# Performance work log

Measured on AMD Instinct MI355X. Metric: run time of the kernel, lower is better.

## Reference

```python
import jax, jax.numpy as jnp
import numpy as np

LOOKBACK = 1
LOOKAHEAD = 0
SEQ, BATCH, IN, HID = 1024, 16, 1024, 1024
K = LOOKBACK + 1 + LOOKAHEAD


def quick_gelu(x):
    return x * jax.nn.sigmoid(1.702 * x)


def setup_inputs() -> dict:
    key = jax.random.key(0)
    ks = jax.random.split(key, 5)
    scale = 1.0 / np.sqrt(IN * K)  # like torch Conv1d default init scale
    X = jax.random.normal(ks[0], (SEQ, BATCH, IN), dtype=jnp.float32)
    Wz = jax.random.normal(ks[1], (HID, IN, K), dtype=jnp.float32) * scale
    bz = jax.random.normal(ks[2], (HID,), dtype=jnp.float32) * scale
    Wf = jax.random.normal(ks[3], (HID, IN, K), dtype=jnp.float32) * scale
    bf = jax.random.normal(ks[4], (HID,), dtype=jnp.float32) * scale
    return {"X": X, "Wz": Wz, "bz": bz, "Wf": Wf, "bf": bf}


def _conv1d(x_pad, W, b):
    # x_pad: (B, Cin, T+K-1), W: (Cout, Cin, K) -> (B, Cout, T)
    y = jax.lax.conv_general_dilated(
        x_pad, W, window_strides=(1,), padding="VALID",
        dimension_numbers=("NCH", "OIH", "NCH"))
    return y + b[None, :, None]


def reference(X, Wz, bz, Wf, bf):
    # pad time dim: lookback zeros before, lookahead zeros after
    X_pad = jnp.pad(X, ((LOOKBACK, LOOKAHEAD), (0, 0), (0, 0)))
    X_pad = jnp.transpose(X_pad, (1, 2, 0))  # (B, Cin, T+K-1)
    Z = jnp.transpose(_conv1d(X_pad, Wz, bz), (2, 0, 1))  # (T, B, H)
    F = jnp.transpose(_conv1d(X_pad, Wf, bf), (2, 0, 1))  # (T, B, H)
    Z = quick_gelu(Z)
    F = jax.nn.sigmoid(F)

    def step(h, fz):
        f, z = fz
        h = f * z + (1.0 - f) * h
        return h, h

    h0 = jnp.zeros((BATCH, HID), dtype=X.dtype)
    _, H = jax.lax.scan(step, h0, (F, Z))  # H: (T, B, HID)
    return H, H[-1:, :, :]
```

## Files before the change

kernel.cpp:

```cpp
#include <hip/hip_runtime.h>
#include <stdint.h>

#define T_SEQ 1024
#define B_SZ  16
#define C_IN  1024
#define C_HID 1024
#define M_ROWS (T_SEQ * B_SZ)
#define N_COLS (2 * C_HID)
#define K_DIM  (2 * C_IN)

#define NCHUNK 16
#define CLEN   (T_SEQ / NCHUNK)
#define NBH    (B_SZ * C_HID)

typedef __attribute__((ext_vector_type(8))) short bf16x8;
typedef __attribute__((ext_vector_type(4))) float f32x4;
typedef unsigned short u16;

#define MFMA __builtin_amdgcn_mfma_f32_16x16x32_bf16

__device__ __forceinline__ u16 f2bf(float f) {
  union { float f; unsigned u; } v; v.f = f;
  unsigned r = v.u + 0x7fffu + ((v.u >> 16) & 1u);
  return (u16)(r >> 16);
}
__device__ __forceinline__ float bf2f(unsigned s) {
  union { unsigned u; float f; } v; v.u = s << 16;
  return v.f;
}

__device__ __forceinline__ void async_cp16(const u16* g, u16* l) {
  __builtin_amdgcn_global_load_lds(
      (const __attribute__((address_space(1))) unsigned*)(uintptr_t)g,
      (__attribute__((address_space(3))) unsigned*)(uintptr_t)l,
      16, 0, 0);
}

__global__ void k_convert_x(const float* __restrict__ X, u16* __restrict__ Xp) {
  int i = blockIdx.x * 256 + threadIdx.x;
  const int total4 = (M_ROWS + B_SZ) * C_IN / 4;
  if (i >= total4) return;
  int e = i << 2;
  const int PAD = B_SZ * C_IN;
  ushort4 o;
  if (e < PAD) {
    o.x = o.y = o.z = o.w = 0;
  } else {
    float4 v = *reinterpret_cast<const float4*>(X + (e - PAD));
    o.x = f2bf(v.x); o.y = f2bf(v.y); o.z = f2bf(v.z); o.w = f2bf(v.w);
  }
  *reinterpret_cast<ushort4*>(Xp + e) = o;
}

__global__ void k_repack_w(const float* __restrict__ Wz, const float* __restrict__ Wf,
                           u16* __restrict__ Wt) {
  int i = blockIdx.x * 256 + threadIdx.x;
  if (i >= 2 * 1024 * 1024) return;
  int g  = i >> 20;
  int hc = i & ((1 << 20) - 1);
  int h  = hc >> 10;
  int c  = hc & 1023;
  const float* W = g ? Wf : Wz;
  float2 w = *reinterpret_cast<const float2*>(W + ((size_t)(h << 10) + c) * 2);
  size_t n = ((size_t)h << 1) | (size_t)g;
  Wt[n * K_DIM + c]        = f2bf(w.x);
  Wt[n * K_DIM + 1024 + c] = f2bf(w.y);
}

__global__ __launch_bounds__(512, 2) void k_gemm8(const u16* __restrict__ Xp,
                                                  const u16* __restrict__ Wt,
                                                  const float* __restrict__ bz,
                                                  const float* __restrict__ bfv,
                                                  u16* __restrict__ Cb) {
  __shared__ u16 lds[2][2][2][8192];
  const int tid  = threadIdx.x;
  const int lane = tid & 63;
  const int wid  = tid >> 6;
  const int wr = wid >> 2;
  const int wc = wid & 3;
  const int lr = lane & 15;

  int wg = (blockIdx.x & 7) * 64 + (blockIdx.x >> 3);
  const int m0 = (wg >> 3) << 8;
  const int n0 = (wg & 7) << 8;

  const int p    = tid << 4;
  const int q    = p ^ (((p >> 7) & 7) << 4);
  const int grow = q >> 7;
  const int gcol = (q & 127) >> 1;
  const int ldsw = (tid >> 6) << 9;

  const int rbase = lr << 6;
  int co[2];
#pragma unroll
  for (int ks = 0; ks < 2; ++ks)
    co[ks] = ((((ks << 6) | ((lane >> 4) << 4)) ^ ((lr & 7) << 4)) >> 1);

  auto stage = [&](int j) {
    int kt = j >> 2, part = j & 3, buf = kt & 1;
    if (part >= 2) {
      int h = part - 2;
      const u16* g = Xp + (size_t)(m0 + (h << 7) + grow + ((kt >= 16) ? B_SZ : 0)) * C_IN
                        + ((kt & 15) << 6) + gcol;
      u16* l = &lds[buf][0][h][ldsw];
      async_cp16(g, l);
      async_cp16(g + (size_t)64 * C_IN, l + 4096);
    } else {
      const u16* g = Wt + (size_t)(n0 + (part << 7) + grow) * K_DIM + (kt << 6) + gcol;
      u16* l = &lds[buf][1][part][ldsw];
      async_cp16(g, l);
      async_cp16(g + (size_t)64 * K_DIM, l + 4096);
    }
  };

  f32x4 acc[8][4] = {};
  bf16x8 a[4][2], b0[2][2], b1[2][2];

  for (int j = 0; j < 7; ++j) stage(j);
  asm volatile("s_waitcnt vmcnt(6)" ::: "memory");
  __builtin_amdgcn_s_barrier();

#pragma unroll 2
  for (int t = 0; t < 32; ++t) {
    const int buf = t & 1;
    const u16* pA = &lds[buf][0][wr][0];
    const u16* pB = &lds[buf][1][wc >> 1][(wc & 1) << 12];
    const int jb = 4 * t + 7;

#pragma unroll
    for (int mi = 0; mi < 4; ++mi)
#pragma unroll
      for (int ks = 0; ks < 2; ++ks)
        a[mi][ks] = *(const bf16x8*)(pA + (mi << 10) + rbase + co[ks]);
#pragma unroll
    for (int ni = 0; ni < 2; ++ni)
#pragma unroll
      for (int ks = 0; ks < 2; ++ks)
        b0[ni][ks] = *(const bf16x8*)(pB + (ni << 10) + rbase + co[ks]);
    if (jb < 128) stage(jb);
    __builtin_amdgcn_s_barrier();
    asm volatile("s_waitcnt lgkmcnt(0)" ::: "memory");
    __builtin_amdgcn_s_setprio(1);
#pragma unroll
    for (int mi = 0; mi < 4; ++mi)
#pragma unroll
      for (int ni = 0; ni < 2; ++ni)
#pragma unroll
        for (int ks = 0; ks < 2; ++ks)
          acc[mi][ni] = MFMA(a[mi][ks], b0[ni][ks], acc[mi][ni], 0, 0, 0);
    __builtin_amdgcn_s_setprio(0);
    __builtin_amdgcn_s_barrier();

#pragma unroll
    for (int ni = 0; ni < 2; ++ni)
#pragma unroll
      for (int ks = 0; ks < 2; ++ks)
        b1[ni][ks] = *(const bf16x8*)(pB + ((2 + ni) << 10) + rbase + co[ks]);
    if (jb + 1 < 128) stage(jb + 1);
    __builtin_amdgcn_s_barrier();
    asm volatile("s_waitcnt lgkmcnt(0)" ::: "memory");
    __builtin_amdgcn_s_setprio(1);
#pragma unroll
    for (int mi = 0; mi < 4; ++mi)
#pragma unroll
      for (int ni = 0; ni < 2; ++ni)
#pragma unroll
        for (int ks = 0; ks < 2; ++ks)
          acc[mi][2 + ni] = MFMA(a[mi][ks], b1[ni][ks], acc[mi][2 + ni], 0, 0, 0);
    __builtin_amdgcn_s_setprio(0);
    __builtin_amdgcn_s_barrier();

#pragma unroll
    for (int mi = 0; mi < 4; ++mi)
#pragma unroll
      for (int ks = 0; ks < 2; ++ks)
        a[mi][ks] = *(const bf16x8*)(pA + ((4 + mi) << 10) + rbase + co[ks]);
    if (jb + 2 < 128) stage(jb + 2);
    __builtin_amdgcn_s_barrier();
    asm volatile("s_waitcnt lgkmcnt(0)" ::: "memory");
    __builtin_amdgcn_s_setprio(1);
#pragma unroll
    for (int mi = 0; mi < 4; ++mi)
#pragma unroll
      for (int ni = 0; ni < 2; ++ni)
#pragma unroll
        for (int ks = 0; ks < 2; ++ks)
          acc[4 + mi][2 + ni] = MFMA(a[mi][ks], b1[ni][ks], acc[4 + mi][2 + ni], 0, 0, 0);
    __builtin_amdgcn_s_setprio(0);
    __builtin_amdgcn_s_barrier();

    if (jb + 3 < 128) stage(jb + 3);
    if (t < 30) asm volatile("s_waitcnt vmcnt(6)" ::: "memory");
    else        asm volatile("s_waitcnt vmcnt(0)" ::: "memory");
    __builtin_amdgcn_s_barrier();
    __builtin_amdgcn_s_setprio(1);
#pragma unroll
    for (int mi = 0; mi < 4; ++mi)
#pragma unroll
      for (int ni = 0; ni < 2; ++ni)
#pragma unroll
        for (int ks = 0; ks < 2; ++ks)
          acc[4 + mi][ni] = MFMA(a[mi][ks], b0[ni][ks], acc[4 + mi][ni], 0, 0, 0);
    __builtin_amdgcn_s_setprio(0);
    __builtin_amdgcn_s_barrier();
  }

  const int erow = (lane >> 4) << 2;
  const int ecol = lane & 15;
#pragma unroll
  for (int ni = 0; ni < 4; ++ni) {
    int col  = n0 + (wc << 6) + (ni << 4) + ecol;
    int hcol = col >> 1;
    bool isz = (col & 1) == 0;
    float bias = isz ? bz[hcol] : bfv[hcol];
    float kk   = isz ? 1.702f : 1.0f;
#pragma unroll
    for (int mi = 0; mi < 8; ++mi) {
      int row = m0 + (wr << 7) + (mi << 4) + erow;
#pragma unroll
      for (int r = 0; r < 4; ++r) {
        float v = acc[mi][ni][r] + bias;
        float s = 1.f / (1.f + __expf(-kk * v));
        float res = isz ? v * s : s;
        Cb[(size_t)(row + r) * N_COLS + col] = f2bf(res);
      }
    }
  }
}

__global__ __launch_bounds__(256) void k_scan1(const u16* __restrict__ Cb,
                                               float* __restrict__ Ap,
                                               float* __restrict__ Bp) {
  int i = blockIdx.x * 256 + threadIdx.x;
  int h = i & (C_HID - 1);
  int b = (i >> 10) & (B_SZ - 1);
  int c = i >> 14;
  const unsigned* Cu = (const unsigned*)Cb;
  size_t base = (size_t)b * C_HID + h + (size_t)c * CLEN * NBH;
  float hh = 0.f, P = 1.f;
#pragma unroll 16
  for (int t = 0; t < CLEN; ++t) {
    unsigned zf = Cu[base + (size_t)t * NBH];
    float z = bf2f(zf & 0xffffu);
    float f = bf2f(zf >> 16);
    hh += f * (z - hh);
    P  *= (1.f - f);
  }
  Ap[i] = hh;
  Bp[i] = P;
}

__global__ __launch_bounds__(256) void k_scan2(const float* __restrict__ Ap,
                                               const float* __restrict__ Bp,
                                               float* __restrict__ St) {
  int i = blockIdx.x * 256 + threadIdx.x;
  float hh = 0.f;
#pragma unroll
  for (int c = 0; c < NCHUNK; ++c) {
    St[c * NBH + i] = hh;
    hh = Ap[c * NBH + i] + Bp[c * NBH + i] * hh;
  }
}

__global__ __launch_bounds__(256) void k_scan3(const u16* __restrict__ Cb,
                                               const float* __restrict__ St,
                                               float* __restrict__ out) {
  int i = blockIdx.x * 256 + threadIdx.x;
  int bh = i & (NBH - 1);
  int c = i >> 14;
  const unsigned* Cu = (const unsigned*)Cb;
  size_t base = (size_t)bh + (size_t)c * CLEN * NBH;
  float hh = St[i];
#pragma unroll 16
  for (int t = 0; t < CLEN; ++t) {
    unsigned zf = Cu[base + (size_t)t * NBH];
    float z = bf2f(zf & 0xffffu);
    float f = bf2f(zf >> 16);
    hh += f * (z - hh);
    out[base + (size_t)t * NBH] = hh;
  }
  if (c == NCHUNK - 1)
    out[(size_t)M_ROWS * C_HID + bh] = hh;
}

extern "C" void kernel_launch(void* const* d_in, const int* in_sizes, int n_in,
                              void* d_out, int out_size, void* d_ws, size_t ws_size,
                              hipStream_t stream) {
  const float* X   = (const float*)d_in[0];
  const float* Wz  = (const float*)d_in[1];
  const float* bz  = (const float*)d_in[2];
  const float* Wf  = (const float*)d_in[3];
  const float* bf_ = (const float*)d_in[4];
  float* out = (float*)d_out;

  u16* Xp = (u16*)d_ws;
  u16* Wt = Xp + (size_t)(M_ROWS + B_SZ) * C_IN;
  u16* Cb = Wt + (size_t)N_COLS * K_DIM;
  float* Ap = (float*)Xp;
  float* Bp = Ap + NCHUNK * NBH;
  float* St = Bp + NCHUNK * NBH;

  hipLaunchKernelGGL(k_convert_x, dim3(16400), dim3(256), 0, stream, X, Xp);
  hipLaunchKernelGGL(k_repack_w, dim3(8192), dim3(256), 0, stream, Wz, Wf, Wt);
  hipLaunchKernelGGL(k_gemm8, dim3((M_ROWS / 256) * (N_COLS / 256)), dim3(512), 0,
                     stream, Xp, Wt, bz, bf_, Cb);
  hipLaunchKernelGGL(k_scan1, dim3(NCHUNK * NBH / 256), dim3(256), 0, stream,
                     Cb, Ap, Bp);
  hipLaunchKernelGGL(k_scan2, dim3(NBH / 256), dim3(256), 0, stream, Ap, Bp, St);
  hipLaunchKernelGGL(k_scan3, dim3(NCHUNK * NBH / 256), dim3(256), 0, stream,
                     Cb, St, out);
}
```

Baseline: 308.1 us.

## Store GEMM output in MFMA fragment layout and vectorize scan reads

```diff
diff --git a/kernel.cpp b/kernel.cpp
--- a/kernel.cpp
+++ b/kernel.cpp
@@ -205,25 +205,26 @@
     __builtin_amdgcn_s_barrier();
   }
 
-  const int erow = (lane >> 4) << 2;
-  const int ecol = lane & 15;
+  const int colp = lane & 15;
+  const bool isz = (colp & 1) == 0;
+  const float kk = isz ? 1.702f : 1.0f;
+  const int hbase = (n0 + (wc << 6) + colp) >> 1;
+  const int fmb = (m0 >> 4) + (wr << 3);
+  const int fnb = (n0 >> 4) + (wc << 2);
 #pragma unroll
   for (int ni = 0; ni < 4; ++ni) {
-    int col  = n0 + (wc << 6) + (ni << 4) + ecol;
-    int hcol = col >> 1;
-    bool isz = (col & 1) == 0;
-    float bias = isz ? bz[hcol] : bfv[hcol];
-    float kk   = isz ? 1.702f : 1.0f;
+    float bias = isz ? bz[hbase + 8 * ni] : bfv[hbase + 8 * ni];
 #pragma unroll
     for (int mi = 0; mi < 8; ++mi) {
-      int row = m0 + (wr << 7) + (mi << 4) + erow;
+      ushort4 o;
 #pragma unroll
       for (int r = 0; r < 4; ++r) {
         float v = acc[mi][ni][r] + bias;
         float s = 1.f / (1.f + __expf(-kk * v));
-        float res = isz ? v * s : s;
-        Cb[(size_t)(row + r) * N_COLS + col] = f2bf(res);
+        ((u16*)&o)[r] = f2bf(isz ? v * s : s);
       }
+      size_t fi = (size_t)(fmb + mi) * 128 + (fnb + ni);
+      *reinterpret_cast<ushort4*>(Cb + fi * 256 + (lane << 2)) = o;
     }
   }
 }
@@ -232,33 +233,42 @@
                                                float* __restrict__ Ap,
                                                float* __restrict__ Bp) {
   int i = blockIdx.x * 256 + threadIdx.x;
-  int h = i & (C_HID - 1);
-  int b = (i >> 10) & (B_SZ - 1);
-  int c = i >> 14;
-  const unsigned* Cu = (const unsigned*)Cb;
-  size_t base = (size_t)b * C_HID + h + (size_t)c * CLEN * NBH;
-  float hh = 0.f, P = 1.f;
-#pragma unroll 16
-  for (int t = 0; t < CLEN; ++t) {
-    unsigned zf = Cu[base + (size_t)t * NBH];
-    float z = bf2f(zf & 0xffffu);
-    float f = bf2f(zf >> 16);
-    hh += f * (z - hh);
-    P  *= (1.f - f);
-  }
-  Ap[i] = hh;
-  Bp[i] = P;
+  int h  = i & (C_HID - 1);
+  int b4 = (i >> 10) & 3;
+  int c  = i >> 12;
+  const size_t lane_off = (size_t)(h >> 3) * 256 + b4 * 64 + (h & 7) * 8;
+  float hh[4] = {0.f, 0.f, 0.f, 0.f}, P[4] = {1.f, 1.f, 1.f, 1.f};
+#pragma unroll 8
+  for (int tt = 0; tt < CLEN; ++tt) {
+    size_t t = (size_t)c * CLEN + tt;
+    uint4 v = *reinterpret_cast<const uint4*>(Cb + t * 32768 + lane_off);
+    float z[4] = {bf2f(v.x & 0xffffu), bf2f(v.x >> 16),
+                  bf2f(v.y & 0xffffu), bf2f(v.y >> 16)};
+    float f[4] = {bf2f(v.z & 0xffffu), bf2f(v.z >> 16),
+                  bf2f(v.w & 0xffffu), bf2f(v.w >> 16)};
+#pragma unroll
+    for (int r = 0; r < 4; ++r) {
+      hh[r] += f[r] * (z[r] - hh[r]);
+      P[r]  *= (1.f - f[r]);
+    }
+  }
+  *reinterpret_cast<f32x4*>(Ap + (size_t)i * 4) = (f32x4){hh[0], hh[1], hh[2], hh[3]};
+  *reinterpret_cast<f32x4*>(Bp + (size_t)i * 4) = (f32x4){P[0], P[1], P[2], P[3]};
 }
 
 __global__ __launch_bounds__(256) void k_scan2(const float* __restrict__ Ap,
                                                const float* __restrict__ Bp,
                                                float* __restrict__ St) {
-  int i = blockIdx.x * 256 + threadIdx.x;
-  float hh = 0.f;
+  int j = blockIdx.x * 256 + threadIdx.x;
+  float hh[4] = {0.f, 0.f, 0.f, 0.f};
 #pragma unroll
   for (int c = 0; c < NCHUNK; ++c) {
-    St[c * NBH + i] = hh;
-    hh = Ap[c * NBH + i] + Bp[c * NBH + i] * hh;
+    size_t idx = ((size_t)c * 4096 + j) * 4;
+    *reinterpret_cast<f32x4*>(St + idx) = (f32x4){hh[0], hh[1], hh[2], hh[3]};
+    f32x4 A = *reinterpret_cast<const f32x4*>(Ap + idx);
+    f32x4 B = *reinterpret_cast<const f32x4*>(Bp + idx);
+#pragma unroll
+    for (int r = 0; r < 4; ++r) hh[r] = A[r] + B[r] * hh[r];
   }
 }
 
@@ -266,21 +276,32 @@
                                                const float* __restrict__ St,
                                                float* __restrict__ out) {
   int i = blockIdx.x * 256 + threadIdx.x;
-  int bh = i & (NBH - 1);
-  int c = i >> 14;
-  const unsigned* Cu = (const unsigned*)Cb;
-  size_t base = (size_t)bh + (size_t)c * CLEN * NBH;
-  float hh = St[i];
-#pragma unroll 16
-  for (int t = 0; t < CLEN; ++t) {
-    unsigned zf = Cu[base + (size_t)t * NBH];
-    float z = bf2f(zf & 0xffffu);
-    float f = bf2f(zf >> 16);
-    hh += f * (z - hh);
-    out[base + (size_t)t * NBH] = hh;
-  }
-  if (c == NCHUNK - 1)
-    out[(size_t)M_ROWS * C_HID + bh] = hh;
+  int h  = i & (C_HID - 1);
+  int b4 = (i >> 10) & 3;
+  int c  = i >> 12;
+  const size_t lane_off = (size_t)(h >> 3) * 256 + b4 * 64 + (h & 7) * 8;
+  f32x4 s = *reinterpret_cast<const f32x4*>(St + (size_t)i * 4);
+  float hh[4] = {s[0], s[1], s[2], s[3]};
+#pragma unroll 8
+  for (int tt = 0; tt < CLEN; ++tt) {
+    size_t t = (size_t)c * CLEN + tt;
+    uint4 v = *reinterpret_cast<const uint4*>(Cb + t * 32768 + lane_off);
+    float z[4] = {bf2f(v.x & 0xffffu), bf2f(v.x >> 16),
+                  bf2f(v.y & 0xffffu), bf2f(v.y >> 16)};
+    float f[4] = {bf2f(v.z & 0xffffu), bf2f(v.z >> 16),
+                  bf2f(v.w & 0xffffu), bf2f(v.w >> 16)};
+    float* op = out + t * 16384 + (size_t)b4 * 4096 + h;
+#pragma unroll
+    for (int r = 0; r < 4; ++r) {
+      hh[r] += f[r] * (z[r] - hh[r]);
+      op[r * 1024] = hh[r];
+    }
+  }
+  if (c == NCHUNK - 1) {
+    float* tp = out + (size_t)M_ROWS * C_HID + (size_t)b4 * 4096 + h;
+#pragma unroll
+    for (int r = 0; r < 4; ++r) tp[r * 1024] = hh[r];
+  }
 }
 
 extern "C" void kernel_launch(void* const* d_in, const int* in_sizes, int n_in,
@@ -297,16 +318,14 @@
   u16* Wt = Xp + (size_t)(M_ROWS + B_SZ) * C_IN;
   u16* Cb = Wt + (size_t)N_COLS * K_DIM;
   float* Ap = (float*)Xp;
-  float* Bp = Ap + NCHUNK * NBH;
-  float* St = Bp + NCHUNK * NBH;
+  float* Bp = Ap + (size_t)NCHUNK * NBH;
+  float* St = Bp + (size_t)NCHUNK * NBH;
 
   hipLaunchKernelGGL(k_convert_x, dim3(16400), dim3(256), 0, stream, X, Xp);
   hipLaunchKernelGGL(k_repack_w, dim3(8192), dim3(256), 0, stream, Wz, Wf, Wt);
   hipLaunchKernelGGL(k_gemm8, dim3((M_ROWS / 256) * (N_COLS / 256)), dim3(512), 0,
                      stream, Xp, Wt, bz, bf_, Cb);
-  hipLaunchKernelGGL(k_scan1, dim3(NCHUNK * NBH / 256), dim3(256), 0, stream,
-                     Cb, Ap, Bp);
-  hipLaunchKernelGGL(k_scan2, dim3(NBH / 256), dim3(256), 0, stream, Ap, Bp, St);
-  hipLaunchKernelGGL(k_scan3, dim3(NCHUNK * NBH / 256), dim3(256), 0, stream,
-                     Cb, St, out);
-}
+  hipLaunchKernelGGL(k_scan1, dim3(256), dim3(256), 0, stream, Cb, Ap, Bp);
+  hipLaunchKernelGGL(k_scan2, dim3(16), dim3(256), 0, stream, Ap, Bp, St);
+  hipLaunchKernelGGL(k_scan3, dim3(256), dim3(256), 0, stream, Cb, St, out);
+}
```

New measurement: 296.9 us. -3.6%, faster.
